# Kernel optimization log

Measured on AMD Instinct MI355X. Metric: run time of the kernel, lower is better.

## Reference

```python
import jax, jax.numpy as jnp
import numpy as np

BN_EPS = 1e-5
N_OUT, D_OUT = 64, 128


def setup_inputs() -> dict:
    key = jax.random.key(0)
    k1, k2, k3, k4 = jax.random.split(key, 4)
    B, N_in, D_in, K = 512, 64, 128, 4
    x = jax.random.normal(k1, (B, N_in, D_in), dtype=jnp.float32)
    # block-sparse weights: one (D_in x D_out) block per (output-row, active-input-row) pair
    W = jax.random.normal(k2, (N_OUT, K, D_in, D_OUT), dtype=jnp.float32) * (1.0 / np.sqrt(K * D_in))
    bias = jax.random.normal(k3, (N_OUT, D_OUT), dtype=jnp.float32) * 0.02
    gamma = jnp.ones((N_OUT * D_OUT,), dtype=jnp.float32)
    beta = jnp.zeros((N_OUT * D_OUT,), dtype=jnp.float32)
    idx = jax.random.randint(k4, (N_OUT, K), 0, N_in, dtype=jnp.int32)
    return {"x": x, "W": W, "bias": bias, "gamma": gamma, "beta": beta, "idx": idx}


def reference(x, W, bias, gamma, beta, idx):
    B = x.shape[0]
    # structured-sparse linear: gather active input rows, per-block matmul
    xg = x[:, idx, :]                                   # [B, N_out, K, D_in]
    y = jnp.einsum('bokd,okde->boe', xg, W) + bias      # [B, N_out, D_out]
    # BatchNorm1d (training-mode batch statistics) on flattened features
    yf = y.reshape(B, -1)                               # [B, N_out*D_out]
    mean = jnp.mean(yf, axis=0)
    var = jnp.mean(jnp.square(yf - mean), axis=0)       # biased variance, as in torch BN
    yn = (yf - mean) * jax.lax.rsqrt(var + BN_EPS) * gamma + beta
    # Swish: z * sigmoid(z)
    out = yn * jax.nn.sigmoid(yn)
    return out.reshape(B, N_OUT, D_OUT)
```

## Files before the change

### kernel.cpp

```cpp
#include <hip/hip_runtime.h>


typedef __attribute__((ext_vector_type(8))) __bf16 bf16x8;
typedef __attribute__((ext_vector_type(4))) __bf16 bf16x4;
typedef __attribute__((ext_vector_type(4))) float  f32x4;

#define B_SZ   512
#define N_IN   64
#define D_IN   128
#define N_O    64
#define D_O    128
#define FEAT   (N_O * D_O)
#define LDA    40

__global__ __launch_bounds__(256, 2)
void gemm_stats_kernel(const float* __restrict__ x, const float* __restrict__ W,
                       const float* __restrict__ bias, const int* __restrict__ idxp,
                       __bf16* __restrict__ y, float* __restrict__ psum,
                       float* __restrict__ psq)
{
    __shared__ __bf16 Alds[128 * LDA];
    __shared__ __bf16 Blds[128 * LDA];

    const int bx   = blockIdx.x;
    const int o    = bx >> 2;
    const int bt   = bx & 3;
    const int b0   = bt * 128;
    const int tid  = threadIdx.x;
    const int wave = tid >> 6;
    const int lane = tid & 63;
    const int wr   = wave >> 1;
    const int wc   = wave & 1;
    const int lam  = lane & 15;
    const int quad = lane >> 4;

    int rsel[4];
#pragma unroll
    for (int k = 0; k < 4; ++k) rsel[k] = idxp[o * 4 + k];

    const f32x4 zero4 = {0.f, 0.f, 0.f, 0.f};
    f32x4 acc[4][4];
#pragma unroll
    for (int mi = 0; mi < 4; ++mi)
#pragma unroll
        for (int ni = 0; ni < 4; ++ni) acc[mi][ni] = zero4;

    const int m_a = tid >> 1;
    const int ca  = (tid & 1) * 16;

    for (int kk = 0; kk < 16; ++kk) {
        const int kidx = kk >> 2;
        const int d0   = (kk & 3) * 32;
        const int r    = rsel[kidx];

        const float* xa = x + (((b0 + m_a) * N_IN + r) * D_IN + d0 + ca);
        f32x4 xv0 = *(const f32x4*)(xa + 0);
        f32x4 xv1 = *(const f32x4*)(xa + 4);
        f32x4 xv2 = *(const f32x4*)(xa + 8);
        f32x4 xv3 = *(const f32x4*)(xa + 12);
        bf16x8 p0, p1;
        p0[0] = (__bf16)xv0[0]; p0[1] = (__bf16)xv0[1];
        p0[2] = (__bf16)xv0[2]; p0[3] = (__bf16)xv0[3];
        p0[4] = (__bf16)xv1[0]; p0[5] = (__bf16)xv1[1];
        p0[6] = (__bf16)xv1[2]; p0[7] = (__bf16)xv1[3];
        p1[0] = (__bf16)xv2[0]; p1[1] = (__bf16)xv2[1];
        p1[2] = (__bf16)xv2[2]; p1[3] = (__bf16)xv2[3];
        p1[4] = (__bf16)xv3[0]; p1[5] = (__bf16)xv3[1];
        p1[6] = (__bf16)xv3[2]; p1[7] = (__bf16)xv3[3];

        bf16x4 wb[4];
        int te[4], tdg[4];
#pragma unroll
        for (int it = 0; it < 4; ++it) {
            const int task = it * 256 + tid;
            const int e  = task & 127;
            const int dg = task >> 7;
            te[it] = e; tdg[it] = dg;
            const float* wp = W + (((o * 4 + kidx) * 128 + (d0 + dg * 4)) * 128 + e);
            wb[it][0] = (__bf16)wp[0];
            wb[it][1] = (__bf16)wp[128];
            wb[it][2] = (__bf16)wp[256];
            wb[it][3] = (__bf16)wp[384];
        }

        __syncthreads();
        *(bf16x8*)&Alds[m_a * LDA + ca]     = p0;
        *(bf16x8*)&Alds[m_a * LDA + ca + 8] = p1;
#pragma unroll
        for (int it = 0; it < 4; ++it)
            *(bf16x4*)&Blds[te[it] * LDA + tdg[it] * 4] = wb[it];
        __syncthreads();

        bf16x8 af[4], bfv[4];
#pragma unroll
        for (int mi = 0; mi < 4; ++mi)
            af[mi] = *(const bf16x8*)&Alds[(wr * 64 + mi * 16 + lam) * LDA + quad * 8];
#pragma unroll
        for (int ni = 0; ni < 4; ++ni)
            bfv[ni] = *(const bf16x8*)&Blds[(wc * 64 + ni * 16 + lam) * LDA + quad * 8];
#pragma unroll
        for (int mi = 0; mi < 4; ++mi)
#pragma unroll
            for (int ni = 0; ni < 4; ++ni)
                acc[mi][ni] = __builtin_amdgcn_mfma_f32_16x16x32_bf16(
                    af[mi], bfv[ni], acc[mi][ni], 0, 0, 0);
    }

    const int nbase = wc * 64;
    float bvals[4];
#pragma unroll
    for (int ni = 0; ni < 4; ++ni)
        bvals[ni] = bias[o * 128 + nbase + ni * 16 + lam];

#pragma unroll
    for (int mi = 0; mi < 4; ++mi)
#pragma unroll
        for (int ni = 0; ni < 4; ++ni)
#pragma unroll
            for (int rr = 0; rr < 4; ++rr) acc[mi][ni][rr] += bvals[ni];

#pragma unroll
    for (int mi = 0; mi < 4; ++mi) {
        const int mrow = b0 + wr * 64 + mi * 16 + quad * 4;
#pragma unroll
        for (int ni = 0; ni < 4; ++ni) {
            const int col = o * 128 + nbase + ni * 16 + lam;
#pragma unroll
            for (int rr = 0; rr < 4; ++rr)
                y[(mrow + rr) * FEAT + col] = (__bf16)acc[mi][ni][rr];
        }
    }

#pragma unroll
    for (int ni = 0; ni < 4; ++ni) {
        float s = 0.f, q = 0.f;
#pragma unroll
        for (int mi = 0; mi < 4; ++mi)
#pragma unroll
            for (int rr = 0; rr < 4; ++rr) {
                const float v = acc[mi][ni][rr];
                s += v; q += v * v;
            }
        s += __shfl_xor(s, 16); s += __shfl_xor(s, 32);
        q += __shfl_xor(q, 16); q += __shfl_xor(q, 32);
        if (quad == 0) {
            const int slot = bt * 2 + wr;
            const int e    = nbase + ni * 16 + lam;
            psum[(o * 8 + slot) * 128 + e] = s;
            psq [(o * 8 + slot) * 128 + e] = q;
        }
    }
}

__global__ __launch_bounds__(256, 4)
void norm_silu_kernel(const __bf16* __restrict__ y, const float* __restrict__ psum,
                      const float* __restrict__ psq, const float* __restrict__ gamma,
                      const float* __restrict__ beta, float* __restrict__ out)
{
    __shared__ float sscale[128];
    __shared__ float sshift[128];
    const int o   = blockIdx.x >> 3;
    const int bc  = blockIdx.x & 7;
    const int tid = threadIdx.x;

    if (tid < 128) {
        float s = 0.f, q = 0.f;
#pragma unroll
        for (int sl = 0; sl < 8; ++sl) {
            s += psum[(o * 8 + sl) * 128 + tid];
            q += psq [(o * 8 + sl) * 128 + tid];
        }
        const float mean = s * (1.0f / 512.0f);
        const float var  = q * (1.0f / 512.0f) - mean * mean;
        const float rstd = rsqrtf(var + 1e-5f);
        const float sc   = rstd * gamma[o * 128 + tid];
        sscale[tid] = sc;
        sshift[tid] = beta[o * 128 + tid] - mean * sc;
    }
    __syncthreads();

#pragma unroll
    for (int it = 0; it < 8; ++it) {
        const int lin = it * 1024 + tid * 4;
        const int bl  = lin >> 7;
        const int e   = lin & 127;
        const int g   = (bc * 64 + bl) * FEAT + o * 128 + e;
        bf16x4 y4 = *(const bf16x4*)&y[g];
        f32x4 ov;
#pragma unroll
        for (int j = 0; j < 4; ++j) {
            const float v  = (float)y4[j];
            const float xn = v * sscale[e + j] + sshift[e + j];
            const float sg = 1.0f / (1.0f + __expf(-xn));
            ov[j] = xn * sg;
        }
        *(f32x4*)&out[g] = ov;
    }
}

extern "C" void kernel_launch(void* const* d_in, const int* in_sizes, int n_in,
                              void* d_out, int out_size, void* d_ws, size_t ws_size,
                              hipStream_t stream)
{
    const float* x     = (const float*)d_in[0];
    const float* W     = (const float*)d_in[1];
    const float* bias  = (const float*)d_in[2];
    const float* gamma = (const float*)d_in[3];
    const float* beta  = (const float*)d_in[4];
    const int*   idx   = (const int*)d_in[5];
    float* out = (float*)d_out;

    __bf16* y   = (__bf16*)d_ws;
    float* psum = (float*)((char*)d_ws + (size_t)B_SZ * FEAT * sizeof(__bf16));
    float* psq  = psum + 64 * 8 * 128;

    gemm_stats_kernel<<<dim3(256), dim3(256), 0, stream>>>(x, W, bias, idx, y, psum, psq);
    norm_silu_kernel<<<dim3(512), dim3(256), 0, stream>>>(y, psum, psq, gamma, beta, out);
}
```

Baseline: 107.5 us.

## Halve GEMM batch tile to 64 rows and widen norm kernel loads to 8 elements

The GEMM kernel now covers 64 batch rows per block instead of 128, which doubles the grid to 512 blocks. Each wave takes a 64x32 output slice, and the stats slots map one per block. This puts more blocks across the CUs, but every block loads and converts the full W tile, so W traffic and conversion work double. Separately, the norm kernel reads 8 bf16 per thread and computes swish as xn/(1+exp(-xn)), cutting load instructions.

```diff
diff --git a/kernel.cpp b/kernel.cpp
--- a/kernel.cpp
+++ b/kernel.cpp
@@ -19,18 +19,16 @@
                        __bf16* __restrict__ y, float* __restrict__ psum,
                        float* __restrict__ psq)
 {
-    __shared__ __bf16 Alds[128 * LDA];
+    __shared__ __bf16 Alds[64 * LDA];
     __shared__ __bf16 Blds[128 * LDA];
 
     const int bx   = blockIdx.x;
-    const int o    = bx >> 2;
-    const int bt   = bx & 3;
-    const int b0   = bt * 128;
+    const int o    = bx >> 3;
+    const int bt   = bx & 7;
+    const int b0   = bt * 64;
     const int tid  = threadIdx.x;
     const int wave = tid >> 6;
     const int lane = tid & 63;
-    const int wr   = wave >> 1;
-    const int wc   = wave & 1;
     const int lam  = lane & 15;
     const int quad = lane >> 4;
 
@@ -39,14 +37,14 @@
     for (int k = 0; k < 4; ++k) rsel[k] = idxp[o * 4 + k];
 
     const f32x4 zero4 = {0.f, 0.f, 0.f, 0.f};
-    f32x4 acc[4][4];
+    f32x4 acc[4][2];
 #pragma unroll
     for (int mi = 0; mi < 4; ++mi)
 #pragma unroll
-        for (int ni = 0; ni < 4; ++ni) acc[mi][ni] = zero4;
-
-    const int m_a = tid >> 1;
-    const int ca  = (tid & 1) * 16;
+        for (int ni = 0; ni < 2; ++ni) acc[mi][ni] = zero4;
+
+    const int m_a = tid >> 2;
+    const int ca  = (tid & 3) * 8;
 
     for (int kk = 0; kk < 16; ++kk) {
         const int kidx = kk >> 2;
@@ -56,17 +54,11 @@
         const float* xa = x + (((b0 + m_a) * N_IN + r) * D_IN + d0 + ca);
         f32x4 xv0 = *(const f32x4*)(xa + 0);
         f32x4 xv1 = *(const f32x4*)(xa + 4);
-        f32x4 xv2 = *(const f32x4*)(xa + 8);
-        f32x4 xv3 = *(const f32x4*)(xa + 12);
-        bf16x8 p0, p1;
+        bf16x8 p0;
         p0[0] = (__bf16)xv0[0]; p0[1] = (__bf16)xv0[1];
         p0[2] = (__bf16)xv0[2]; p0[3] = (__bf16)xv0[3];
         p0[4] = (__bf16)xv1[0]; p0[5] = (__bf16)xv1[1];
         p0[6] = (__bf16)xv1[2]; p0[7] = (__bf16)xv1[3];
-        p1[0] = (__bf16)xv2[0]; p1[1] = (__bf16)xv2[1];
-        p1[2] = (__bf16)xv2[2]; p1[3] = (__bf16)xv2[3];
-        p1[4] = (__bf16)xv3[0]; p1[5] = (__bf16)xv3[1];
-        p1[6] = (__bf16)xv3[2]; p1[7] = (__bf16)xv3[3];
 
         bf16x4 wb[4];
         int te[4], tdg[4];
@@ -84,46 +76,45 @@
         }
 
         __syncthreads();
-        *(bf16x8*)&Alds[m_a * LDA + ca]     = p0;
-        *(bf16x8*)&Alds[m_a * LDA + ca + 8] = p1;
+        *(bf16x8*)&Alds[m_a * LDA + ca] = p0;
 #pragma unroll
         for (int it = 0; it < 4; ++it)
             *(bf16x4*)&Blds[te[it] * LDA + tdg[it] * 4] = wb[it];
         __syncthreads();
 
-        bf16x8 af[4], bfv[4];
+        bf16x8 af[4], bfv[2];
 #pragma unroll
         for (int mi = 0; mi < 4; ++mi)
-            af[mi] = *(const bf16x8*)&Alds[(wr * 64 + mi * 16 + lam) * LDA + quad * 8];
-#pragma unroll
-        for (int ni = 0; ni < 4; ++ni)
-            bfv[ni] = *(const bf16x8*)&Blds[(wc * 64 + ni * 16 + lam) * LDA + quad * 8];
+            af[mi] = *(const bf16x8*)&Alds[(mi * 16 + lam) * LDA + quad * 8];
+#pragma unroll
+        for (int ni = 0; ni < 2; ++ni)
+            bfv[ni] = *(const bf16x8*)&Blds[(wave * 32 + ni * 16 + lam) * LDA + quad * 8];
 #pragma unroll
         for (int mi = 0; mi < 4; ++mi)
 #pragma unroll
-            for (int ni = 0; ni < 4; ++ni)
+            for (int ni = 0; ni < 2; ++ni)
                 acc[mi][ni] = __builtin_amdgcn_mfma_f32_16x16x32_bf16(
                     af[mi], bfv[ni], acc[mi][ni], 0, 0, 0);
     }
 
-    const int nbase = wc * 64;
-    float bvals[4];
-#pragma unroll
-    for (int ni = 0; ni < 4; ++ni)
+    const int nbase = wave * 32;
+    float bvals[2];
+#pragma unroll
+    for (int ni = 0; ni < 2; ++ni)
         bvals[ni] = bias[o * 128 + nbase + ni * 16 + lam];
 
 #pragma unroll
     for (int mi = 0; mi < 4; ++mi)
 #pragma unroll
-        for (int ni = 0; ni < 4; ++ni)
+        for (int ni = 0; ni < 2; ++ni)
 #pragma unroll
             for (int rr = 0; rr < 4; ++rr) acc[mi][ni][rr] += bvals[ni];
 
 #pragma unroll
     for (int mi = 0; mi < 4; ++mi) {
-        const int mrow = b0 + wr * 64 + mi * 16 + quad * 4;
-#pragma unroll
-        for (int ni = 0; ni < 4; ++ni) {
+        const int mrow = b0 + mi * 16 + quad * 4;
+#pragma unroll
+        for (int ni = 0; ni < 2; ++ni) {
             const int col = o * 128 + nbase + ni * 16 + lam;
 #pragma unroll
             for (int rr = 0; rr < 4; ++rr)
@@ -132,7 +123,7 @@
     }
 
 #pragma unroll
-    for (int ni = 0; ni < 4; ++ni) {
+    for (int ni = 0; ni < 2; ++ni) {
         float s = 0.f, q = 0.f;
 #pragma unroll
         for (int mi = 0; mi < 4; ++mi)
@@ -144,10 +135,9 @@
         s += __shfl_xor(s, 16); s += __shfl_xor(s, 32);
         q += __shfl_xor(q, 16); q += __shfl_xor(q, 32);
         if (quad == 0) {
-            const int slot = bt * 2 + wr;
-            const int e    = nbase + ni * 16 + lam;
-            psum[(o * 8 + slot) * 128 + e] = s;
-            psq [(o * 8 + slot) * 128 + e] = q;
+            const int e = nbase + ni * 16 + lam;
+            psum[(o * 8 + bt) * 128 + e] = s;
+            psq [(o * 8 + bt) * 128 + e] = q;
         }
     }
 }
@@ -180,21 +170,27 @@
     __syncthreads();
 
 #pragma unroll
-    for (int it = 0; it < 8; ++it) {
-        const int lin = it * 1024 + tid * 4;
+    for (int it = 0; it < 4; ++it) {
+        const int lin = it * 2048 + tid * 8;
         const int bl  = lin >> 7;
         const int e   = lin & 127;
         const int g   = (bc * 64 + bl) * FEAT + o * 128 + e;
-        bf16x4 y4 = *(const bf16x4*)&y[g];
-        f32x4 ov;
+        bf16x8 y8 = *(const bf16x8*)&y[g];
+        f32x4 ov0, ov1;
 #pragma unroll
         for (int j = 0; j < 4; ++j) {
-            const float v  = (float)y4[j];
+            const float v  = (float)y8[j];
             const float xn = v * sscale[e + j] + sshift[e + j];
-            const float sg = 1.0f / (1.0f + __expf(-xn));
-            ov[j] = xn * sg;
-        }
-        *(f32x4*)&out[g] = ov;
+            ov0[j] = xn / (1.0f + __expf(-xn));
+        }
+#pragma unroll
+        for (int j = 0; j < 4; ++j) {
+            const float v  = (float)y8[4 + j];
+            const float xn = v * sscale[e + 4 + j] + sshift[e + 4 + j];
+            ov1[j] = xn / (1.0f + __expf(-xn));
+        }
+        *(f32x4*)&out[g]     = ov0;
+        *(f32x4*)&out[g + 4] = ov1;
     }
 }
 
@@ -214,6 +210,6 @@
     float* psum = (float*)((char*)d_ws + (size_t)B_SZ * FEAT * sizeof(__bf16));
     float* psq  = psum + 64 * 8 * 128;
 
-    gemm_stats_kernel<<<dim3(256), dim3(256), 0, stream>>>(x, W, bias, idx, y, psum, psq);
+    gemm_stats_kernel<<<dim3(512), dim3(256), 0, stream>>>(x, W, bias, idx, y, psum, psq);
     norm_silu_kernel<<<dim3(512), dim3(256), 0, stream>>>(y, psum, psq, gamma, beta, out);
 }
```

Result: slower. 112.4 us (+4.6%).
